# Optimization experiments

Measured on AMD Instinct MI355X. Metric: run time of the kernel, lower is better.

The kernel has to match this reference:

```python
import jax, jax.numpy as jnp
import numpy as np

B, T, M, D = 4, 512, 16, 128
P, H = 128, 4
E = P // H


def _glorot(k, shape, fan_in, fan_out):
    lim = np.sqrt(6.0 / (fan_in + fan_out)).astype(np.float32)
    return jax.random.uniform(k, shape, jnp.float32, -lim, lim)


def setup_inputs() -> dict:
    key = jax.random.key(0)
    ks = jax.random.split(key, 12)
    inp = jax.random.normal(ks[0], (B, T, M, D), jnp.float32)
    pos = jax.random.normal(ks[1], (B, T, 1, D), jnp.float32)
    # padding mask: valid time steps per batch element (ensures no fully-masked softmax row)
    lengths = jax.random.randint(ks[2], (B,), T // 2, T + 1)
    mask = jnp.broadcast_to(jnp.arange(T)[None, :, None] < lengths[:, None, None], (B, T, M))
    Wq = _glorot(ks[3], (M, P, D), D, P)
    Wk = _glorot(ks[4], (M, P, D), D, P)
    Wv = _glorot(ks[5], (M, P, D), D, P)
    Wq_t = _glorot(ks[6], (M, P, D), D, P)
    Wk_t = _glorot(ks[7], (M, P, D), D, P)
    Bq = jnp.zeros((M, P), jnp.float32)
    Bk = jnp.zeros((M, P), jnp.float32)
    Bv = jnp.zeros((M, P), jnp.float32)
    Bq_t = jnp.zeros((M, P), jnp.float32)
    Bk_t = jnp.zeros((M, P), jnp.float32)
    return {"inp": inp, "pos": pos, "mask": mask,
            "Wq": Wq, "Bq": Bq, "Wk": Wk, "Bk": Bk, "Wv": Wv, "Bv": Bv,
            "Wq_t": Wq_t, "Bq_t": Bq_t, "Wk_t": Wk_t, "Bk_t": Bk_t}


def reference(inp, pos, mask, Wq, Bq, Wk, Bk, Wv, Bv, Wq_t, Bq_t, Wk_t, Bk_t):
    b, t, m, d = inp.shape
    p = Wq.shape[1]
    h, e = H, P // H
    # per-modality projections: (m,p,d) x (b,t,m,d) -> (b,t,m,p)
    q = jnp.einsum('mpd,btmd->btmp', Wq, inp) + Bq
    k = jnp.einsum('mpd,btmd->btmp', Wk, inp) + Bk
    v = jnp.einsum('mpd,btmd->btmp', Wv, inp) + Bv
    pos0 = pos[:, :, 0, :]  # (b,t,d); broadcasts across m
    q_t = jnp.einsum('mpd,btd->btmp', Wq_t, pos0) + Bq_t
    k_t = jnp.einsum('mpd,btd->btmp', Wk_t, pos0) + Bk_t

    def split_heads(x):  # (b,t,m,p) -> (b,m,h,t,e)
        return x.reshape(b, t, m, h, e).transpose(0, 2, 3, 1, 4)

    q, k, v, q_t, k_t = map(split_heads, (q, k, v, q_t, k_t))
    # dual bilinear score: content + positional
    score = (jnp.einsum('bmhte,bmhse->bmhts', q, k)
             + jnp.einsum('bmhte,bmhse->bmhts', q_t, k_t)) / (2.0 * np.sqrt(e).astype(np.float32))
    causal = jnp.tril(jnp.ones((t, t), bool))  # (t,t)
    score = jnp.where(causal, score, -jnp.inf)
    km = mask.transpose(0, 2, 1)[:, :, None, None, :]  # (b,m,1,1,t)
    score = jnp.where(km, score, -jnp.inf)
    w = jax.nn.softmax(score, axis=-1)
    w = jnp.where(km, w, 0.0)
    w = jnp.where(causal, w, 0.0)
    # dropout is identity at inference (drop_rate ignored)
    out = jnp.einsum('bmhts,bmhse->bmhte', w, v)
    return out.transpose(0, 3, 1, 2, 4).reshape(b, t, m, p)
```

## Files before the change

### kernel.cpp

```cpp
#include <hip/hip_runtime.h>

#define Bn 4
#define Tn 512
#define Mn 16
#define Dn 128
#define Pn 128
#define Hn 4
#define SCALE 0.08838834764831845f

typedef unsigned short u16;
typedef unsigned int u32;
typedef short s16;
typedef __attribute__((ext_vector_type(8))) s16 bf16x8;
typedef __attribute__((ext_vector_type(4))) float f32x4;

__device__ __forceinline__ u16 f2b(float f) {
  u32 x; __builtin_memcpy(&x, &f, 4);
  x += 0x7fffu + ((x >> 16) & 1u);
  return (u16)(x >> 16);
}
__device__ __forceinline__ u32 pack2(float a, float b) {
  return (u32)f2b(a) | ((u32)f2b(b) << 16);
}
__device__ __forceinline__ bf16x8 ld8(const u16* p) {
  bf16x8 r; __builtin_memcpy(&r, p, 16); return r;
}
__device__ __forceinline__ f32x4 mfma16(bf16x8 a, bf16x8 b, f32x4 c) {
  return __builtin_amdgcn_mfma_f32_16x16x32_bf16(a, b, c, 0, 0, 0);
}

__global__ void lengths_kernel(const void* __restrict__ mask, int* __restrict__ len_out) {
  const int b = blockIdx.x;
  __shared__ int cnt[256];
  const u32 w0 = ((const u32*)mask)[0];
  const int mode = (w0 == 1u) ? 0 : (w0 == 0x3F800000u) ? 1
                 : (w0 == 0x3F803F80u) ? 2 : 3;
  int c = 0;
  for (int t = threadIdx.x; t < Tn; t += 256) {
    const size_t idx = ((size_t)b * Tn + t) * Mn;
    int nz;
    if (mode == 0)      nz = (((const int*)mask)[idx] != 0);
    else if (mode == 1) nz = (((const u32*)mask)[idx] != 0u);
    else if (mode == 2) nz = (((const u16*)mask)[idx] != 0);
    else                nz = (((const unsigned char*)mask)[idx] != 0);
    c += nz;
  }
  cnt[threadIdx.x] = c;
  __syncthreads();
  for (int s = 128; s > 0; s >>= 1) {
    if (threadIdx.x < (unsigned)s) cnt[threadIdx.x] += cnt[threadIdx.x + s];
    __syncthreads();
  }
  if (threadIdx.x == 0) len_out[b] = cnt[0];
}

__global__ __launch_bounds__(256) void proj_mfma(
    const float* __restrict__ inp, const float* __restrict__ pos,
    const float* __restrict__ Wq, const float* __restrict__ Bq,
    const float* __restrict__ Wk, const float* __restrict__ Bk,
    const float* __restrict__ Wv, const float* __restrict__ Bv,
    const float* __restrict__ Wqt, const float* __restrict__ Bqt,
    const float* __restrict__ Wkt, const float* __restrict__ Bkt,
    u16* __restrict__ Qa, u16* __restrict__ Ka, u16* __restrict__ Qb,
    u16* __restrict__ Kb, u16* __restrict__ Vt) {
  const int tid = threadIdx.x;
  const int bid = blockIdx.x;
  const int tsel = bid % 5;
  const int m = (bid / 5) % Mn;
  const int rt0 = (bid / (5 * Mn)) * 128;

  const float* W; const float* Bb; int usepos, doscale;
  u16* dst;
  switch (tsel) {
    case 0:  W = Wq;  Bb = Bq;  usepos = 0; doscale = 1; dst = Qa; break;
    case 1:  W = Wk;  Bb = Bk;  usepos = 0; doscale = 0; dst = Ka; break;
    case 2:  W = Wv;  Bb = Bv;  usepos = 0; doscale = 0; dst = Vt; break;
    case 3:  W = Wqt; Bb = Bqt; usepos = 1; doscale = 1; dst = Qb; break;
    default: W = Wkt; Bb = Bkt; usepos = 1; doscale = 0; dst = Kb; break;
  }
  const float* A = usepos ? pos : inp;

  __shared__ __align__(16) u16 Xs[128 * 72];
  __shared__ __align__(16) u16 Ws2[128 * 72];

  const int wv = tid >> 6, lane = tid & 63;
  const int quad = lane >> 4, l16 = lane & 15;

  f32x4 acc[2][8];
#pragma unroll
  for (int qs = 0; qs < 2; ++qs)
#pragma unroll
    for (int n = 0; n < 8; ++n) acc[qs][n] = (f32x4){0.f, 0.f, 0.f, 0.f};

  for (int kh = 0; kh < 2; ++kh) {
    for (int idx = tid; idx < 128 * 16; idx += 256) {
      const int row = idx >> 4, c4 = (idx & 15) * 4, col = kh * 64 + c4;
      const size_t sx = usepos ? ((size_t)(rt0 + row) * Dn + col)
                               : (((size_t)(rt0 + row) * Mn + m) * Dn + col);
      const float4 x = *(const float4*)(A + sx);
      ushort4 xh; xh.x = f2b(x.x); xh.y = f2b(x.y); xh.z = f2b(x.z); xh.w = f2b(x.w);
      *(ushort4*)&Xs[row * 72 + c4] = xh;
      const float4 w = *(const float4*)(W + ((size_t)m * Pn + row) * Dn + col);
      ushort4 wh; wh.x = f2b(w.x); wh.y = f2b(w.y); wh.z = f2b(w.z); wh.w = f2b(w.w);
      *(ushort4*)&Ws2[row * 72 + c4] = wh;
    }
    __syncthreads();
#pragma unroll
    for (int kc = 0; kc < 2; ++kc) {
      const int ko = kc * 32 + quad * 8;
      const bf16x8 a0 = ld8(&Xs[(wv * 32 + l16) * 72 + ko]);
      const bf16x8 a1 = ld8(&Xs[(wv * 32 + 16 + l16) * 72 + ko]);
#pragma unroll
      for (int n = 0; n < 8; ++n) {
        const bf16x8 bn = ld8(&Ws2[(n * 16 + l16) * 72 + ko]);
        acc[0][n] = mfma16(a0, bn, acc[0][n]);
        acc[1][n] = mfma16(a1, bn, acc[1][n]);
      }
    }
    __syncthreads();
  }

  const int b = rt0 >> 9;
  const int tl0 = (rt0 & (Tn - 1)) + wv * 32;
#pragma unroll
  for (int n = 0; n < 8; ++n) {
    const int h = n >> 1, e = (n & 1) * 16 + l16;
    const float bias = Bb[m * Pn + n * 16 + l16];
    const int bmh = (b * Mn + m) * Hn + h;
    if (tsel != 2) {
#pragma unroll
      for (int qs = 0; qs < 2; ++qs)
#pragma unroll
        for (int reg = 0; reg < 4; ++reg) {
          const int t = tl0 + qs * 16 + quad * 4 + reg;
          float v = acc[qs][n][reg] + bias;
          if (doscale) v *= SCALE;
          dst[((size_t)bmh * Tn + t) * 32 + e] = f2b(v);
        }
    } else {
      const size_t rowv = ((size_t)bmh * 32 + e) * Tn;
#pragma unroll
      for (int qs = 0; qs < 2; ++qs) {
        const int t0 = tl0 + qs * 16 + quad * 4;
        uint2 d;
        d.x = pack2(acc[qs][n][0] + bias, acc[qs][n][1] + bias);
        d.y = pack2(acc[qs][n][2] + bias, acc[qs][n][3] + bias);
        *(uint2*)&dst[rowv + t0] = d;
      }
    }
  }
}

__global__ __launch_bounds__(256, 4) void attn_flash(
    const u16* __restrict__ Qa, const u16* __restrict__ Ka,
    const u16* __restrict__ Qb, const u16* __restrict__ Kb,
    const u16* __restrict__ Vt, const int* __restrict__ lens,
    float* __restrict__ out) {
  __shared__ __align__(16) u16 Ps[4 * 32 * 72];

  const int tid = threadIdx.x;
  const int wv = tid >> 6, lane = tid & 63;
  const int quad = lane >> 4, l16 = lane & 15;

  const int wu = blockIdx.x * 4 + wv;
  const int qt = wu & 15;
  const int bmh = wu >> 4;
  const int b = bmh >> 6;
  const int len = lens[b];
  const int q0 = qt * 32;

  const size_t rowbase = (size_t)bmh * Tn;
  const size_t vbase = (size_t)bmh * 32 * Tn;
  u16* myPs = &Ps[wv * 32 * 72];

  bf16x8 qf[2][2];
#pragma unroll
  for (int qs = 0; qs < 2; ++qs) {
    const size_t r = (rowbase + q0 + qs * 16 + l16) * 32 + quad * 8;
    qf[qs][0] = ld8(Qa + r);
    qf[qs][1] = ld8(Qb + r);
  }

  f32x4 O[2][2];
#pragma unroll
  for (int qs = 0; qs < 2; ++qs)
#pragma unroll
    for (int es = 0; es < 2; ++es) O[qs][es] = (f32x4){0.f, 0.f, 0.f, 0.f};
  float mrow[2] = {-1e30f, -1e30f}, lsum[2] = {0.f, 0.f};

  const int s_hi = min(q0 + 32, len);
  for (int s0 = 0; s0 < s_hi; s0 += 64) {
    f32x4 S[2][4];
#pragma unroll
    for (int st = 0; st < 4; ++st) {
      const size_t kr = (rowbase + s0 + st * 16 + l16) * 32 + quad * 8;
      const bf16x8 k0 = ld8(Ka + kr);
      const bf16x8 k1 = ld8(Kb + kr);
#pragma unroll
      for (int qs = 0; qs < 2; ++qs)
        S[qs][st] = mfma16(k1, qf[qs][1], mfma16(k0, qf[qs][0],
                           st == -1 ? S[qs][st] : (f32x4){0.f, 0.f, 0.f, 0.f}));
    }

#pragma unroll
    for (int qs = 0; qs < 2; ++qs) {
      const int q = q0 + qs * 16 + l16;
      const int qcap = min(q, len - 1);
      const int sb = s0 + quad * 4;
      float cmax = -1e30f;
#pragma unroll
      for (int st = 0; st < 4; ++st)
#pragma unroll
        for (int reg = 0; reg < 4; ++reg) {
          const int s = sb + st * 16 + reg;
          const float v = (s <= qcap) ? S[qs][st][reg] : -1e30f;
          S[qs][st][reg] = v;
          cmax = fmaxf(cmax, v);
        }
      cmax = fmaxf(cmax, __shfl_xor(cmax, 16));
      cmax = fmaxf(cmax, __shfl_xor(cmax, 32));
      const float mnew = fmaxf(mrow[qs], cmax);
      const float alpha = __expf(mrow[qs] - mnew);
      mrow[qs] = mnew;
      float rsum = 0.f;
      u32 pk[4][2];
#pragma unroll
      for (int st = 0; st < 4; ++st) {
        const float p0 = __expf(S[qs][st][0] - mnew);
        const float p1 = __expf(S[qs][st][1] - mnew);
        const float p2 = __expf(S[qs][st][2] - mnew);
        const float p3 = __expf(S[qs][st][3] - mnew);
        rsum += (p0 + p1) + (p2 + p3);
        pk[st][0] = pack2(p0, p1);
        pk[st][1] = pack2(p2, p3);
      }
      rsum += __shfl_xor(rsum, 16);
      rsum += __shfl_xor(rsum, 32);
      lsum[qs] = lsum[qs] * alpha + rsum;
#pragma unroll
      for (int es = 0; es < 2; ++es)
#pragma unroll
        for (int reg = 0; reg < 4; ++reg) O[qs][es][reg] *= alpha;
#pragma unroll
      for (int st = 0; st < 4; ++st) {
        uint2 d; d.x = pk[st][0]; d.y = pk[st][1];
        *(uint2*)&myPs[(qs * 16 + l16) * 72 + st * 16 + quad * 4] = d;
      }
    }

#pragma unroll
    for (int kc = 0; kc < 2; ++kc) {
      const int ko = kc * 32 + quad * 8;
      const bf16x8 pf0 = ld8(&myPs[l16 * 72 + ko]);
      const bf16x8 pf1 = ld8(&myPs[(16 + l16) * 72 + ko]);
      const bf16x8 vf0 = ld8(Vt + vbase + (size_t)l16 * Tn + s0 + ko);
      const bf16x8 vf1 = ld8(Vt + vbase + (size_t)(16 + l16) * Tn + s0 + ko);
      O[0][0] = mfma16(vf0, pf0, O[0][0]);
      O[0][1] = mfma16(vf1, pf0, O[0][1]);
      O[1][0] = mfma16(vf0, pf1, O[1][0]);
      O[1][1] = mfma16(vf1, pf1, O[1][1]);
    }
  }

  const int mm = (bmh >> 2) & (Mn - 1);
  const int h = bmh & (Hn - 1);
#pragma unroll
  for (int qs = 0; qs < 2; ++qs) {
    const float linv = 1.0f / lsum[qs];
    const int t = q0 + qs * 16 + l16;
    const size_t ob = (((size_t)b * Tn + t) * Mn + mm) * Pn + h * 32 + quad * 4;
#pragma unroll
    for (int es = 0; es < 2; ++es) {
      float4 o;
      o.x = O[qs][es][0] * linv; o.y = O[qs][es][1] * linv;
      o.z = O[qs][es][2] * linv; o.w = O[qs][es][3] * linv;
      *(float4*)&out[ob + es * 16] = o;
    }
  }
}

extern "C" void kernel_launch(void* const* d_in, const int* in_sizes, int n_in,
                              void* d_out, int out_size, void* d_ws, size_t ws_size,
                              hipStream_t stream) {
  const float* inp = (const float*)d_in[0];
  const float* pos = (const float*)d_in[1];
  const void* mask = d_in[2];
  const float* Wq  = (const float*)d_in[3];
  const float* Bq  = (const float*)d_in[4];
  const float* Wk  = (const float*)d_in[5];
  const float* Bk  = (const float*)d_in[6];
  const float* Wv  = (const float*)d_in[7];
  const float* Bv  = (const float*)d_in[8];
  const float* Wqt = (const float*)d_in[9];
  const float* Bqt = (const float*)d_in[10];
  const float* Wkt = (const float*)d_in[11];
  const float* Bkt = (const float*)d_in[12];
  float* out = (float*)d_out;

  const size_t nA = (size_t)Bn * Mn * Hn * Tn * 32;
  u16* Qa = (u16*)d_ws;
  u16* Ka = Qa + nA;
  u16* Qb = Ka + nA;
  u16* Kb = Qb + nA;
  u16* Vt = Kb + nA;
  int* lens = (int*)(Vt + nA);

  lengths_kernel<<<Bn, 256, 0, stream>>>(mask, lens);
  proj_mfma<<<(Bn * Tn / 128) * Mn * 5, 256, 0, stream>>>(
      inp, pos, Wq, Bq, Wk, Bk, Wv, Bv, Wqt, Bqt, Wkt, Bkt, Qa, Ka, Qb, Kb, Vt);
  attn_flash<<<Bn * Mn * Hn * (Tn / 32) / 4, 256, 0, stream>>>(
      Qa, Ka, Qb, Kb, Vt, lens, out);
}
```

Measured before the change: 151.3 us.

## Pre-convert inputs and weights to bf16 and fuse Q/K/V projections per wave

Adds a separate conversion kernel that casts the input, positional input and all five weight tensors to bf16 once and copies the biases into workspace. The projection kernel now reads the bf16 data straight from global memory, with no LDS staging or block barriers. Each wave computes Q, K and V together, or Q_t and K_t together, so it reads its input tile once instead of once per projection. The aim is to cut repeated fp32 reads and per-block conversion work, at the cost of an extra kernel launch, extra bf16 traffic to and from workspace, and higher register pressure from three accumulator sets.

```diff
diff --git a/kernel.cpp b/kernel.cpp
--- a/kernel.cpp
+++ b/kernel.cpp
@@ -8,6 +8,12 @@
 #define Hn 4
 #define SCALE 0.08838834764831845f
 
+#define N4_INP (Bn * Tn * Mn * Dn / 4)
+#define N4_POS (Bn * Tn * Dn / 4)
+#define N4_W   (Mn * Pn * Dn / 4)
+#define WSZ    (Mn * Pn * Dn)
+#define CVT_BLOCKS ((N4_INP + N4_POS + 5 * N4_W) / 256)
+
 typedef unsigned short u16;
 typedef unsigned int u32;
 typedef short s16;
@@ -28,6 +34,7 @@
 __device__ __forceinline__ f32x4 mfma16(bf16x8 a, bf16x8 b, f32x4 c) {
   return __builtin_amdgcn_mfma_f32_16x16x32_bf16(a, b, c, 0, 0, 0);
 }
+#define ZERO4 ((f32x4){0.f, 0.f, 0.f, 0.f})
 
 __global__ void lengths_kernel(const void* __restrict__ mask, int* __restrict__ len_out) {
   const int b = blockIdx.x;
@@ -54,99 +61,159 @@
   if (threadIdx.x == 0) len_out[b] = cnt[0];
 }
 
-__global__ __launch_bounds__(256) void proj_mfma(
+__global__ __launch_bounds__(256) void cvt_kernel(
     const float* __restrict__ inp, const float* __restrict__ pos,
-    const float* __restrict__ Wq, const float* __restrict__ Bq,
-    const float* __restrict__ Wk, const float* __restrict__ Bk,
-    const float* __restrict__ Wv, const float* __restrict__ Bv,
-    const float* __restrict__ Wqt, const float* __restrict__ Bqt,
-    const float* __restrict__ Wkt, const float* __restrict__ Bkt,
+    const float* __restrict__ Wq, const float* __restrict__ Wk,
+    const float* __restrict__ Wv, const float* __restrict__ Wqt,
+    const float* __restrict__ Wkt,
+    const float* __restrict__ Bq, const float* __restrict__ Bk,
+    const float* __restrict__ Bv, const float* __restrict__ Bqt,
+    const float* __restrict__ Bkt,
+    u16* __restrict__ Xbf, u16* __restrict__ Pbf, u16* __restrict__ Wbf,
+    float* __restrict__ Bws) {
+  const int gb = blockIdx.x;
+  if (gb < CVT_BLOCKS) {
+    const int i = gb * 256 + threadIdx.x;
+    const float* src; u16* dst; int off;
+    if (i < N4_INP) {
+      src = inp; dst = Xbf; off = i;
+    } else if (i < N4_INP + N4_POS) {
+      src = pos; dst = Pbf; off = i - N4_INP;
+    } else {
+      const int w = i - (N4_INP + N4_POS);
+      const int tsel = w >> 16;
+      off = w & 65535;
+      dst = Wbf + tsel * WSZ;
+      src = (tsel == 0) ? Wq : (tsel == 1) ? Wk : (tsel == 2) ? Wv
+          : (tsel == 3) ? Wqt : Wkt;
+    }
+    const float4 v = ((const float4*)src)[off];
+    ushort4 o;
+    o.x = f2b(v.x); o.y = f2b(v.y); o.z = f2b(v.z); o.w = f2b(v.w);
+    ((ushort4*)dst)[off] = o;
+  } else {
+    for (int i = threadIdx.x; i < 5 * Mn * Pn; i += 256) {
+      const int arr = i >> 11, idx = i & 2047;
+      const float* src = (arr == 0) ? Bq : (arr == 1) ? Bk : (arr == 2) ? Bv
+                       : (arr == 3) ? Bqt : Bkt;
+      Bws[i] = src[idx];
+    }
+  }
+}
+
+__global__ __launch_bounds__(256, 2) void proj_mfma(
+    const u16* __restrict__ Xbf, const u16* __restrict__ Pbf,
+    const u16* __restrict__ Wbf, const float* __restrict__ Bws,
     u16* __restrict__ Qa, u16* __restrict__ Ka, u16* __restrict__ Qb,
     u16* __restrict__ Kb, u16* __restrict__ Vt) {
   const int tid = threadIdx.x;
-  const int bid = blockIdx.x;
-  const int tsel = bid % 5;
-  const int m = (bid / 5) % Mn;
-  const int rt0 = (bid / (5 * Mn)) * 128;
-
-  const float* W; const float* Bb; int usepos, doscale;
-  u16* dst;
-  switch (tsel) {
-    case 0:  W = Wq;  Bb = Bq;  usepos = 0; doscale = 1; dst = Qa; break;
-    case 1:  W = Wk;  Bb = Bk;  usepos = 0; doscale = 0; dst = Ka; break;
-    case 2:  W = Wv;  Bb = Bv;  usepos = 0; doscale = 0; dst = Vt; break;
-    case 3:  W = Wqt; Bb = Bqt; usepos = 1; doscale = 1; dst = Qb; break;
-    default: W = Wkt; Bb = Bkt; usepos = 1; doscale = 0; dst = Kb; break;
-  }
-  const float* A = usepos ? pos : inp;
-
-  __shared__ __align__(16) u16 Xs[128 * 72];
-  __shared__ __align__(16) u16 Ws2[128 * 72];
-
   const int wv = tid >> 6, lane = tid & 63;
   const int quad = lane >> 4, l16 = lane & 15;
-
-  f32x4 acc[2][8];
-#pragma unroll
-  for (int qs = 0; qs < 2; ++qs)
-#pragma unroll
-    for (int n = 0; n < 8; ++n) acc[qs][n] = (f32x4){0.f, 0.f, 0.f, 0.f};
-
-  for (int kh = 0; kh < 2; ++kh) {
-    for (int idx = tid; idx < 128 * 16; idx += 256) {
-      const int row = idx >> 4, c4 = (idx & 15) * 4, col = kh * 64 + c4;
-      const size_t sx = usepos ? ((size_t)(rt0 + row) * Dn + col)
-                               : (((size_t)(rt0 + row) * Mn + m) * Dn + col);
-      const float4 x = *(const float4*)(A + sx);
-      ushort4 xh; xh.x = f2b(x.x); xh.y = f2b(x.y); xh.z = f2b(x.z); xh.w = f2b(x.w);
-      *(ushort4*)&Xs[row * 72 + c4] = xh;
-      const float4 w = *(const float4*)(W + ((size_t)m * Pn + row) * Dn + col);
-      ushort4 wh; wh.x = f2b(w.x); wh.y = f2b(w.y); wh.z = f2b(w.z); wh.w = f2b(w.w);
-      *(ushort4*)&Ws2[row * 72 + c4] = wh;
-    }
-    __syncthreads();
-#pragma unroll
-    for (int kc = 0; kc < 2; ++kc) {
+  const int wu = blockIdx.x * 4 + wv;
+
+  const int isqkv = (wu < 1024);
+  const int wu2 = isqkv ? wu : wu - 1024;
+  const int rg = wu2 & 63;
+  const int m = wu2 >> 6;
+  const int bt0 = rg * 32;
+  const int tl = bt0 & (Tn - 1);
+  const int b = bt0 >> 9;
+  const int bmh0 = (b * Mn + m) * Hn;
+
+  if (isqkv) {
+    const u16* Wqp = Wbf + 0 * WSZ + m * Pn * Dn;
+    const u16* Wkp = Wbf + 1 * WSZ + m * Pn * Dn;
+    const u16* Wvp = Wbf + 2 * WSZ + m * Pn * Dn;
+    f32x4 accQ[2][8], accK[2][8], accV[2][8];
+#pragma unroll
+    for (int tt = 0; tt < 2; ++tt)
+#pragma unroll
+      for (int n = 0; n < 8; ++n) {
+        accQ[tt][n] = ZERO4; accK[tt][n] = ZERO4; accV[tt][n] = ZERO4;
+      }
+#pragma unroll
+    for (int kc = 0; kc < 4; ++kc) {
       const int ko = kc * 32 + quad * 8;
-      const bf16x8 a0 = ld8(&Xs[(wv * 32 + l16) * 72 + ko]);
-      const bf16x8 a1 = ld8(&Xs[(wv * 32 + 16 + l16) * 72 + ko]);
+      const bf16x8 x0 = ld8(Xbf + ((size_t)(bt0 + l16) * Mn + m) * Dn + ko);
+      const bf16x8 x1 = ld8(Xbf + ((size_t)(bt0 + 16 + l16) * Mn + m) * Dn + ko);
 #pragma unroll
       for (int n = 0; n < 8; ++n) {
-        const bf16x8 bn = ld8(&Ws2[(n * 16 + l16) * 72 + ko]);
-        acc[0][n] = mfma16(a0, bn, acc[0][n]);
-        acc[1][n] = mfma16(a1, bn, acc[1][n]);
-      }
-    }
-    __syncthreads();
-  }
-
-  const int b = rt0 >> 9;
-  const int tl0 = (rt0 & (Tn - 1)) + wv * 32;
-#pragma unroll
-  for (int n = 0; n < 8; ++n) {
-    const int h = n >> 1, e = (n & 1) * 16 + l16;
-    const float bias = Bb[m * Pn + n * 16 + l16];
-    const int bmh = (b * Mn + m) * Hn + h;
-    if (tsel != 2) {
-#pragma unroll
-      for (int qs = 0; qs < 2; ++qs)
+        const size_t wr = (size_t)(n * 16 + l16) * Dn + ko;
+        const bf16x8 wq = ld8(Wqp + wr);
+        const bf16x8 wk = ld8(Wkp + wr);
+        const bf16x8 wvv = ld8(Wvp + wr);
+        accQ[0][n] = mfma16(x0, wq, accQ[0][n]);
+        accQ[1][n] = mfma16(x1, wq, accQ[1][n]);
+        accK[0][n] = mfma16(x0, wk, accK[0][n]);
+        accK[1][n] = mfma16(x1, wk, accK[1][n]);
+        accV[0][n] = mfma16(x0, wvv, accV[0][n]);
+        accV[1][n] = mfma16(x1, wvv, accV[1][n]);
+      }
+    }
+#pragma unroll
+    for (int n = 0; n < 8; ++n) {
+      const int p = n * 16 + l16;
+      const int h = p >> 5, e = p & 31;
+      const int bmh = bmh0 + h;
+      const float bq = Bws[0 * 2048 + m * Pn + p];
+      const float bk = Bws[1 * 2048 + m * Pn + p];
+      const float bv = Bws[2 * 2048 + m * Pn + p];
+#pragma unroll
+      for (int tt = 0; tt < 2; ++tt) {
 #pragma unroll
         for (int reg = 0; reg < 4; ++reg) {
-          const int t = tl0 + qs * 16 + quad * 4 + reg;
-          float v = acc[qs][n][reg] + bias;
-          if (doscale) v *= SCALE;
-          dst[((size_t)bmh * Tn + t) * 32 + e] = f2b(v);
+          const int t = tl + tt * 16 + quad * 4 + reg;
+          const size_t ad = ((size_t)bmh * Tn + t) * 32 + e;
+          Qa[ad] = f2b((accQ[tt][n][reg] + bq) * SCALE);
+          Ka[ad] = f2b(accK[tt][n][reg] + bk);
         }
-    } else {
-      const size_t rowv = ((size_t)bmh * 32 + e) * Tn;
-#pragma unroll
-      for (int qs = 0; qs < 2; ++qs) {
-        const int t0 = tl0 + qs * 16 + quad * 4;
-        uint2 d;
-        d.x = pack2(acc[qs][n][0] + bias, acc[qs][n][1] + bias);
-        d.y = pack2(acc[qs][n][2] + bias, acc[qs][n][3] + bias);
-        *(uint2*)&dst[rowv + t0] = d;
-      }
+        const int t0 = tl + tt * 16 + quad * 4;
+        uint2 dv;
+        dv.x = pack2(accV[tt][n][0] + bv, accV[tt][n][1] + bv);
+        dv.y = pack2(accV[tt][n][2] + bv, accV[tt][n][3] + bv);
+        *(uint2*)&Vt[((size_t)bmh * 32 + e) * Tn + t0] = dv;
+      }
+    }
+  } else {
+    const u16* Wqp = Wbf + 3 * WSZ + m * Pn * Dn;
+    const u16* Wkp = Wbf + 4 * WSZ + m * Pn * Dn;
+    f32x4 accQ[2][8], accK[2][8];
+#pragma unroll
+    for (int tt = 0; tt < 2; ++tt)
+#pragma unroll
+      for (int n = 0; n < 8; ++n) { accQ[tt][n] = ZERO4; accK[tt][n] = ZERO4; }
+#pragma unroll
+    for (int kc = 0; kc < 4; ++kc) {
+      const int ko = kc * 32 + quad * 8;
+      const bf16x8 x0 = ld8(Pbf + (size_t)(bt0 + l16) * Dn + ko);
+      const bf16x8 x1 = ld8(Pbf + (size_t)(bt0 + 16 + l16) * Dn + ko);
+#pragma unroll
+      for (int n = 0; n < 8; ++n) {
+        const size_t wr = (size_t)(n * 16 + l16) * Dn + ko;
+        const bf16x8 wq = ld8(Wqp + wr);
+        const bf16x8 wk = ld8(Wkp + wr);
+        accQ[0][n] = mfma16(x0, wq, accQ[0][n]);
+        accQ[1][n] = mfma16(x1, wq, accQ[1][n]);
+        accK[0][n] = mfma16(x0, wk, accK[0][n]);
+        accK[1][n] = mfma16(x1, wk, accK[1][n]);
+      }
+    }
+#pragma unroll
+    for (int n = 0; n < 8; ++n) {
+      const int p = n * 16 + l16;
+      const int h = p >> 5, e = p & 31;
+      const int bmh = bmh0 + h;
+      const float bq = Bws[3 * 2048 + m * Pn + p];
+      const float bk = Bws[4 * 2048 + m * Pn + p];
+#pragma unroll
+      for (int tt = 0; tt < 2; ++tt)
+#pragma unroll
+        for (int reg = 0; reg < 4; ++reg) {
+          const int t = tl + tt * 16 + quad * 4 + reg;
+          const size_t ad = ((size_t)bmh * Tn + t) * 32 + e;
+          Qb[ad] = f2b((accQ[tt][n][reg] + bq) * SCALE);
+          Kb[ad] = f2b(accK[tt][n][reg] + bk);
+        }
     }
   }
 }
@@ -185,7 +252,7 @@
 #pragma unroll
   for (int qs = 0; qs < 2; ++qs)
 #pragma unroll
-    for (int es = 0; es < 2; ++es) O[qs][es] = (f32x4){0.f, 0.f, 0.f, 0.f};
+    for (int es = 0; es < 2; ++es) O[qs][es] = ZERO4;
   float mrow[2] = {-1e30f, -1e30f}, lsum[2] = {0.f, 0.f};
 
   const int s_hi = min(q0 + 32, len);
@@ -198,8 +265,7 @@
       const bf16x8 k1 = ld8(Kb + kr);
 #pragma unroll
       for (int qs = 0; qs < 2; ++qs)
-        S[qs][st] = mfma16(k1, qf[qs][1], mfma16(k0, qf[qs][0],
-                           st == -1 ? S[qs][st] : (f32x4){0.f, 0.f, 0.f, 0.f}));
+        S[qs][st] = mfma16(k1, qf[qs][1], mfma16(k0, qf[qs][0], ZERO4));
     }
 
 #pragma unroll
@@ -303,11 +369,17 @@
   u16* Qb = Ka + nA;
   u16* Kb = Qb + nA;
   u16* Vt = Kb + nA;
-  int* lens = (int*)(Vt + nA);
+  u16* Xbf = Vt + nA;
+  u16* Pbf = Xbf + (size_t)Bn * Tn * Mn * Dn;
+  u16* Wbf = Pbf + (size_t)Bn * Tn * Dn;
+  float* Bws = (float*)(Wbf + 5 * (size_t)WSZ);
+  int* lens = (int*)(Bws + 5 * 2048);
 
   lengths_kernel<<<Bn, 256, 0, stream>>>(mask, lens);
-  proj_mfma<<<(Bn * Tn / 128) * Mn * 5, 256, 0, stream>>>(
-      inp, pos, Wq, Bq, Wk, Bk, Wv, Bv, Wqt, Bqt, Wkt, Bkt, Qa, Ka, Qb, Kb, Vt);
+  cvt_kernel<<<CVT_BLOCKS + 1, 256, 0, stream>>>(
+      inp, pos, Wq, Wk, Wv, Wqt, Wkt, Bq, Bk, Bv, Bqt, Bkt,
+      Xbf, Pbf, Wbf, Bws);
+  proj_mfma<<<2048 / 4, 256, 0, stream>>>(Xbf, Pbf, Wbf, Bws, Qa, Ka, Qb, Kb, Vt);
   attn_flash<<<Bn * Mn * Hn * (Tn / 32) / 4, 256, 0, stream>>>(
       Qa, Ka, Qb, Kb, Vt, lens, out);
 }
```

New measurement: 182.9 us. +20.9%, slower.
